# Optimization experiments

Hardware: AMD Instinct MI355X
Metric: run time of the kernel (lower is better)

## Reference

```python
import jax, jax.numpy as jnp
import numpy as np

D_MODEL = 1024


def bitlinear(x, weight):
    # ternary quantization with straight-through estimator; forward value is w_q*scale
    scale = jnp.clip(jnp.mean(jnp.abs(weight), axis=1, keepdims=True), 1e-5, None)
    w_q = jnp.clip(jnp.round(weight / scale), -1.0, 1.0)
    w = weight + jax.lax.stop_gradient(w_q * scale - weight)
    return x @ w.T


def rmsnorm(x, w, eps=1e-6):
    return x * jax.lax.rsqrt(jnp.mean(x * x, axis=-1, keepdims=True) + eps) * w


def setup_inputs() -> dict:
    key = jax.random.key(0)
    ks = jax.random.split(key, 6)
    D = D_MODEL
    std = np.sqrt(2.0 / D)  # kaiming_normal fan_out
    return {
        "x": jax.random.normal(ks[0], (4, 4096, D), dtype=jnp.float32),
        "Wr": jax.random.normal(ks[1], (D, D), dtype=jnp.float32) * std,
        "Wk": jax.random.normal(ks[2], (D, D), dtype=jnp.float32) * std,
        "Wv": jax.random.normal(ks[3], (D, D), dtype=jnp.float32) * std,
        "Wo": jax.random.normal(ks[4], (D, D), dtype=jnp.float32) * std,
        "decay": jnp.ones((D,), dtype=jnp.float32) * 0.99,
        "ln_w": jnp.ones((D,), dtype=jnp.float32),
    }


def reference(x, Wr, Wk, Wv, Wo, decay, ln_w):
    B, T, D = x.shape
    r = jax.nn.sigmoid(bitlinear(x, Wr))
    k = bitlinear(x, Wk)
    v = bitlinear(x, Wv)
    dec = jax.nn.sigmoid(decay)                              # [D]
    kv = k * v                                               # [B,T,D]
    positions = jnp.arange(T, dtype=x.dtype)                 # [T]
    log_decay = jnp.log(jnp.clip(dec, 1e-7, None))           # [D]
    scale = jnp.exp(positions[:, None] * log_decay[None, :])  # [T,D]
    scaled = kv / jnp.clip(scale, 1e-10, None)[None]         # [B,T,D]
    cum = jnp.cumsum(scaled, axis=1)                         # [B,T,D]
    state = cum * scale[None]                                # [B,T,D]
    return bitlinear(rmsnorm(r * state, ln_w), Wo)
```

## Files before the change

### kernel.cpp

```cpp
#include <hip/hip_runtime.h>

typedef unsigned short u16;
typedef __attribute__((ext_vector_type(8))) short bf16x8;
typedef __attribute__((ext_vector_type(4))) float f32x4;
typedef __attribute__((ext_vector_type(4))) unsigned short u16x4;

#define DM 1024

__device__ __forceinline__ float bf2f(u16 u){
  union { unsigned int i; float f; } v; v.i = ((unsigned int)u)<<16; return v.f;
}
__device__ __forceinline__ u16 f2bf(float f){
  unsigned int x = __float_as_uint(f);
  return (u16)((x + 0x7FFFu + ((x>>16)&1u)) >> 16);
}

__global__ __launch_bounds__(256)
void quantize_w(const float* __restrict__ W0, const float* __restrict__ W1,
                const float* __restrict__ W2, const float* __restrict__ W3,
                u16* __restrict__ wq, float* __restrict__ wsc)
{
  const int gr   = blockIdx.x*4 + (threadIdx.x>>6);
  const int lane = threadIdx.x & 63;
  const float* W; int row;
  if (gr < 1024)      { W = W0; row = gr; }
  else if (gr < 3072) { row = (gr-1024)>>1; W = (gr&1) ? W2 : W1; }
  else                { W = W3; row = gr-3072; }
  const float* wr = W + (size_t)row*DM;
  float4 v[4]; float s = 0.f;
  #pragma unroll
  for (int c=0;c<4;c++){
    v[c] = *(const float4*)&wr[c*256 + lane*4];
    s += fabsf(v[c].x)+fabsf(v[c].y)+fabsf(v[c].z)+fabsf(v[c].w);
  }
  #pragma unroll
  for (int off=32; off; off>>=1) s += __shfl_down(s, off);
  s = __shfl(s, 0);
  const float scale = fmaxf(s*(1.f/1024.f), 1e-5f);
  if (lane==0) wsc[gr] = scale;
  u16* wo = wq + (size_t)gr*DM;
  #pragma unroll
  for (int c=0;c<4;c++){
    u16x4 q;
    q[0] = f2bf(fminf(fmaxf(rintf(v[c].x/scale),-1.f),1.f));
    q[1] = f2bf(fminf(fmaxf(rintf(v[c].y/scale),-1.f),1.f));
    q[2] = f2bf(fminf(fmaxf(rintf(v[c].z/scale),-1.f),1.f));
    q[3] = f2bf(fminf(fmaxf(rintf(v[c].w/scale),-1.f),1.f));
    *(u16x4*)&wo[c*256 + lane*4] = q;
  }
}

__global__ void cvt_x(const float* __restrict__ x, u16* __restrict__ xb){
  const int i = (blockIdx.x*256 + threadIdx.x)*4;
  float4 v = *(const float4*)&x[i];
  u16x4 o; o[0]=f2bf(v.x); o[1]=f2bf(v.y); o[2]=f2bf(v.z); o[3]=f2bf(v.w);
  *(u16x4*)&xb[i] = o;
}


#define RD(base, off) (*(const bf16x8*)((const char*)(base) + (off)))

template<int MODE>
__global__ __launch_bounds__(256, 4)
void gemm_s(const u16* __restrict__ Ag, const u16* __restrict__ Bq,
            const float* __restrict__ bscale,
            u16* __restrict__ o_r, u16* __restrict__ o_kv,
            float* __restrict__ o_f)
{
  __shared__ u16 sA[128*64];
  __shared__ u16 sB[128*64];
  const int tid = threadIdx.x, wave = tid>>6, lane = tid&63;
  const int lr = lane&15, lg = lane>>4;
  const int wm = wave>>1, wn = wave&1;
  const int bm0 = blockIdx.x*128, bn0 = blockIdx.y*128;
  constexpr int nt = 16;

  const int r8   = lane>>3;
  const int scol = ((lane&7)<<4) ^ (r8<<4);
  const size_t aoff = (size_t)(bm0 + wave*8 + r8)*2048 + scol;
  const size_t boff = (size_t)(bn0 + wave*8 + r8)*2048 + scol;
  const int ldst = wave*1024;

  const int S = (lr&7)<<4;
  const int koff0 = ((lg<<4)     ) ^ S;
  const int koff1 = (64 + (lg<<4)) ^ S;
  const int arow = (wm*64 + lr)*128;
  const int brow = (wn*64 + lr)*128;

  f32x4 acc[4][4];
  #pragma unroll
  for (int i=0;i<4;i++)
    #pragma unroll
    for (int j=0;j<4;j++) acc[i][j] = (f32x4){0.f,0.f,0.f,0.f};

  for (int t=0; t<nt; ++t){
    #pragma unroll
    for (int q=0;q<4;q++){
      __builtin_amdgcn_global_load_lds(
        (const __attribute__((address_space(1))) void*)((const char*)Ag + aoff + q*65536 + (size_t)t*128),
        (__attribute__((address_space(3))) void*)((char*)sA + ldst + q*4096), 16, 0, 0);
      __builtin_amdgcn_global_load_lds(
        (const __attribute__((address_space(1))) void*)((const char*)Bq + boff + q*65536 + (size_t)t*128),
        (__attribute__((address_space(3))) void*)((char*)sB + ldst + q*4096), 16, 0, 0);
    }
    __syncthreads();
    {
      bf16x8 a[4], b[4];
      #pragma unroll
      for (int m=0;m<4;m++) a[m] = RD(sA, arow + m*2048 + koff0);
      #pragma unroll
      for (int n=0;n<4;n++) b[n] = RD(sB, brow + n*2048 + koff0);
      #pragma unroll
      for (int m=0;m<4;m++)
        #pragma unroll
        for (int n=0;n<4;n++)
          acc[m][n] = __builtin_amdgcn_mfma_f32_16x16x32_bf16(a[m], b[n], acc[m][n], 0,0,0);
      #pragma unroll
      for (int m=0;m<4;m++) a[m] = RD(sA, arow + m*2048 + koff1);
      #pragma unroll
      for (int n=0;n<4;n++) b[n] = RD(sB, brow + n*2048 + koff1);
      #pragma unroll
      for (int m=0;m<4;m++)
        #pragma unroll
        for (int n=0;n<4;n++)
          acc[m][n] = __builtin_amdgcn_mfma_f32_16x16x32_bf16(a[m], b[n], acc[m][n], 0,0,0);
    }
    __syncthreads();
  }

  #pragma unroll
  for (int mi=0; mi<4; ++mi){
    #pragma unroll
    for (int ni=0; ni<4; ++ni){
      const int col = bn0 + wn*64 + ni*16 + lr;
      const float sc = bscale[col];
      const int rowb = bm0 + wm*64 + mi*16 + lg*4;
      const f32x4 a = acc[mi][ni];
      if (MODE==0){
        if (bn0 < 1024){
          #pragma unroll
          for (int r2=0;r2<4;r2++){
            const float val = a[r2]*sc;
            o_r[(size_t)(rowb+r2)*DM + col] = f2bf(1.f/(1.f+expf(-val)));
          }
        } else {
          const int dv = (col - 1024) >> 1;
          #pragma unroll
          for (int r2=0;r2<4;r2++){
            const float val = a[r2]*sc;
            const float pr  = val * __shfl_xor(val, 1);
            if (!(lr & 1))
              o_kv[(size_t)(rowb+r2)*DM + dv] = f2bf(pr);
          }
        }
      } else {
        #pragma unroll
        for (int r2=0;r2<4;r2++)
          o_f[(size_t)(rowb+r2)*DM + col] = a[r2]*sc;
      }
    }
  }
}

__global__ __launch_bounds__(256)
void kv_phase1(const u16* __restrict__ kv, const float* __restrict__ decay,
               float* __restrict__ part)
{
  const int c = blockIdx.x & 127, b = blockIdx.x >> 7;
  const int d0 = threadIdx.x*4;
  float ld[4]; f32x4 sum = {0.f,0.f,0.f,0.f};
  #pragma unroll
  for (int j=0;j<4;j++){
    const float dec = 1.f/(1.f+expf(-decay[d0+j]));
    ld[j] = logf(fmaxf(dec, 1e-7f));
  }
  for (int t=c*32; t<c*32+32; ++t){
    const size_t base = ((size_t)(b*4096 + t))*DM + d0;
    const u16x4 p4 = *(const u16x4*)&kv[base];
    const float tf = (float)t;
    #pragma unroll
    for (int j=0;j<4;j++){
      const float e = expf(tf*ld[j]);
      sum[j] += bf2f(p4[j]) / fmaxf(e, 1e-10f);
    }
  }
  *(f32x4*)&part[((size_t)(b*128+c))*DM + d0] = sum;
}

__global__ void chunk_prefix(float* __restrict__ part){
  const int g = blockIdx.x*256 + threadIdx.x;
  const int b = g >> 8, d0 = (g & 255)*4;
  f32x4 run = {0.f,0.f,0.f,0.f};
  for (int c8=0; c8<128; c8+=8){
    f32x4 v[8];
    #pragma unroll
    for (int i=0;i<8;i++)
      v[i] = *(const f32x4*)&part[((size_t)(b*128+c8+i))*DM + d0];
    #pragma unroll
    for (int i=0;i<8;i++){
      const f32x4 tmp = v[i];
      *(f32x4*)&part[((size_t)(b*128+c8+i))*DM + d0] = run;
      run += tmp;
    }
  }
}

__global__ __launch_bounds__(256)
void scan_norm(const u16* __restrict__ kv, const u16* __restrict__ rbuf,
               const float* __restrict__ part, const float* __restrict__ decay,
               const float* __restrict__ lnw, u16* __restrict__ yn)
{
  const int c = blockIdx.x & 127, b = blockIdx.x >> 7;
  const int tid = threadIdx.x, lane = tid&63, wave = tid>>6;
  const int d0 = tid*4;
  __shared__ float red[2][4];
  f32x4 run = *(const f32x4*)&part[((size_t)(b*128+c))*DM + d0];
  float ld[4], lw[4];
  #pragma unroll
  for (int j=0;j<4;j++){
    const float dec = 1.f/(1.f+expf(-decay[d0+j]));
    ld[j] = logf(fmaxf(dec, 1e-7f));
    lw[j] = lnw[d0+j];
  }
  for (int t=c*32; t<c*32+32; ++t){
    const size_t base = ((size_t)(b*4096+t))*DM + d0;
    const u16x4 p4 = *(const u16x4*)&kv[base];
    const u16x4 r4 = *(const u16x4*)&rbuf[base];
    const float tf = (float)t;
    float y[4]; float ss = 0.f;
    #pragma unroll
    for (int j=0;j<4;j++){
      const float e = expf(tf*ld[j]);
      run[j] += bf2f(p4[j]) / fmaxf(e, 1e-10f);
      const float st = run[j]*e;
      y[j] = bf2f(r4[j])*st;
      ss += y[j]*y[j];
    }
    #pragma unroll
    for (int off=32; off; off>>=1) ss += __shfl_down(ss, off);
    if (lane==0) red[t&1][wave] = ss;
    __builtin_amdgcn_s_barrier();
    const float tot = (red[t&1][0]+red[t&1][1])+(red[t&1][2]+red[t&1][3]);
    const float rs = 1.f/sqrtf(tot*(1.f/1024.f) + 1e-6f);
    u16x4 o;
    #pragma unroll
    for (int j=0;j<4;j++) o[j] = f2bf(y[j]*rs*lw[j]);
    *(u16x4*)&yn[base] = o;
  }
}

extern "C" void kernel_launch(void* const* d_in, const int* in_sizes, int n_in,
                              void* d_out, int out_size, void* d_ws, size_t ws_size,
                              hipStream_t stream)
{
  (void)in_sizes; (void)n_in; (void)out_size; (void)ws_size;
  const float* x    = (const float*)d_in[0];
  const float* Wr   = (const float*)d_in[1];
  const float* Wk   = (const float*)d_in[2];
  const float* Wv   = (const float*)d_in[3];
  const float* Wo   = (const float*)d_in[4];
  const float* dec  = (const float*)d_in[5];
  const float* lnw  = (const float*)d_in[6];

  char* ws = (char*)d_ws;
  u16*   wq     = (u16*)(ws + 0);
  float* wsc    = (float*)(ws + 8388608);
  u16*   rbuf   = (u16*)(ws + 8404992);
  u16*   kvbuf  = (u16*)(ws + 41959424);
  float* part   = (float*)(ws + 75513856);
  u16*   xb     = (u16*)(ws + 77611008);
  u16*   yn     = (u16*)(ws + 111165440);

  quantize_w<<<1024, 256, 0, stream>>>(Wr, Wk, Wv, Wo, wq, wsc);
  cvt_x<<<16384, 256, 0, stream>>>(x, xb);
  gemm_s<0><<<dim3(128,24), 256, 0, stream>>>(xb, wq, wsc, rbuf, kvbuf, nullptr);
  kv_phase1<<<512, 256, 0, stream>>>(kvbuf, dec, part);
  chunk_prefix<<<4, 256, 0, stream>>>(part);
  scan_norm<<<512, 256, 0, stream>>>(kvbuf, rbuf, part, dec, lnw, yn);
  gemm_s<1><<<dim3(128,8), 256, 0, stream>>>(yn, wq + 3*1024*1024, wsc + 3072,
                                             nullptr, nullptr, (float*)d_out);
}
```

Baseline: 242.2 us.

## Quantize normalized activations to int8 and run output projection with int8 MFMA

The output projection now uses int8 ternary weights and per-row absmax int8-quantized activations, produced directly by the scan/norm kernel along with a per-row scale. It runs on a new int8 MFMA GEMM (16x16x64) with half the bytes per K step. The aim is to cut the final GEMM's load traffic and MFMA count and to shrink the yn write. It also widens the chunk prefix kernel to one scalar column per thread across more blocks. The cost is extra quantization error on activations (int8 vs bf16), which could affect tolerance.

```diff
diff --git a/kernel.cpp b/kernel.cpp
--- a/kernel.cpp
+++ b/kernel.cpp
@@ -3,6 +3,7 @@
 typedef unsigned short u16;
 typedef __attribute__((ext_vector_type(8))) short bf16x8;
 typedef __attribute__((ext_vector_type(4))) float f32x4;
+typedef __attribute__((ext_vector_type(4))) int   i32x4;
 typedef __attribute__((ext_vector_type(4))) unsigned short u16x4;
 
 #define DM 1024
@@ -18,7 +19,8 @@
 __global__ __launch_bounds__(256)
 void quantize_w(const float* __restrict__ W0, const float* __restrict__ W1,
                 const float* __restrict__ W2, const float* __restrict__ W3,
-                u16* __restrict__ wq, float* __restrict__ wsc)
+                u16* __restrict__ wq, signed char* __restrict__ wq8,
+                float* __restrict__ wsc)
 {
   const int gr   = blockIdx.x*4 + (threadIdx.x>>6);
   const int lane = threadIdx.x & 63;
@@ -38,15 +40,28 @@
   s = __shfl(s, 0);
   const float scale = fmaxf(s*(1.f/1024.f), 1e-5f);
   if (lane==0) wsc[gr] = scale;
-  u16* wo = wq + (size_t)gr*DM;
-  #pragma unroll
-  for (int c=0;c<4;c++){
-    u16x4 q;
-    q[0] = f2bf(fminf(fmaxf(rintf(v[c].x/scale),-1.f),1.f));
-    q[1] = f2bf(fminf(fmaxf(rintf(v[c].y/scale),-1.f),1.f));
-    q[2] = f2bf(fminf(fmaxf(rintf(v[c].z/scale),-1.f),1.f));
-    q[3] = f2bf(fminf(fmaxf(rintf(v[c].w/scale),-1.f),1.f));
-    *(u16x4*)&wo[c*256 + lane*4] = q;
+  if (gr < 3072){
+    u16* wo = wq + (size_t)gr*DM;
+    #pragma unroll
+    for (int c=0;c<4;c++){
+      u16x4 q;
+      q[0] = f2bf(fminf(fmaxf(rintf(v[c].x/scale),-1.f),1.f));
+      q[1] = f2bf(fminf(fmaxf(rintf(v[c].y/scale),-1.f),1.f));
+      q[2] = f2bf(fminf(fmaxf(rintf(v[c].z/scale),-1.f),1.f));
+      q[3] = f2bf(fminf(fmaxf(rintf(v[c].w/scale),-1.f),1.f));
+      *(u16x4*)&wo[c*256 + lane*4] = q;
+    }
+  } else {
+    signed char* wo = wq8 + (size_t)(gr-3072)*DM;
+    #pragma unroll
+    for (int c=0;c<4;c++){
+      const int q0 = (int)rintf(fminf(fmaxf(v[c].x/scale,-1.f),1.f));
+      const int q1 = (int)rintf(fminf(fmaxf(v[c].y/scale,-1.f),1.f));
+      const int q2 = (int)rintf(fminf(fmaxf(v[c].z/scale,-1.f),1.f));
+      const int q3 = (int)rintf(fminf(fmaxf(v[c].w/scale,-1.f),1.f));
+      const unsigned int p = (q0&0xFF) | ((q1&0xFF)<<8) | ((q2&0xFF)<<16) | ((unsigned)(q3&0xFF)<<24);
+      *(unsigned int*)&wo[c*256 + lane*4] = p;
+    }
   }
 }
 
@@ -57,15 +72,12 @@
   *(u16x4*)&xb[i] = o;
 }
 
-
 #define RD(base, off) (*(const bf16x8*)((const char*)(base) + (off)))
 
-template<int MODE>
 __global__ __launch_bounds__(256, 4)
-void gemm_s(const u16* __restrict__ Ag, const u16* __restrict__ Bq,
-            const float* __restrict__ bscale,
-            u16* __restrict__ o_r, u16* __restrict__ o_kv,
-            float* __restrict__ o_f)
+void gemm_rkv(const u16* __restrict__ Ag, const u16* __restrict__ Bq,
+              const float* __restrict__ bscale,
+              u16* __restrict__ o_r, u16* __restrict__ o_kv)
 {
   __shared__ u16 sA[128*64];
   __shared__ u16 sB[128*64];
@@ -136,28 +148,108 @@
       const float sc = bscale[col];
       const int rowb = bm0 + wm*64 + mi*16 + lg*4;
       const f32x4 a = acc[mi][ni];
-      if (MODE==0){
-        if (bn0 < 1024){
-          #pragma unroll
-          for (int r2=0;r2<4;r2++){
-            const float val = a[r2]*sc;
-            o_r[(size_t)(rowb+r2)*DM + col] = f2bf(1.f/(1.f+expf(-val)));
-          }
-        } else {
-          const int dv = (col - 1024) >> 1;
-          #pragma unroll
-          for (int r2=0;r2<4;r2++){
-            const float val = a[r2]*sc;
-            const float pr  = val * __shfl_xor(val, 1);
-            if (!(lr & 1))
-              o_kv[(size_t)(rowb+r2)*DM + dv] = f2bf(pr);
-          }
+      if (bn0 < 1024){
+        #pragma unroll
+        for (int r2=0;r2<4;r2++){
+          const float val = a[r2]*sc;
+          o_r[(size_t)(rowb+r2)*DM + col] = f2bf(1.f/(1.f+expf(-val)));
         }
       } else {
-        #pragma unroll
-        for (int r2=0;r2<4;r2++)
-          o_f[(size_t)(rowb+r2)*DM + col] = a[r2]*sc;
+        const int dv = (col - 1024) >> 1;
+        #pragma unroll
+        for (int r2=0;r2<4;r2++){
+          const float val = a[r2]*sc;
+          const float pr  = val * __shfl_xor(val, 1);
+          if (!(lr & 1))
+            o_kv[(size_t)(rowb+r2)*DM + dv] = f2bf(pr);
+        }
       }
+    }
+  }
+}
+
+#define RD8(base, off) (*(const i32x4*)((const char*)(base) + (off)))
+
+__global__ __launch_bounds__(256, 4)
+void gemm_o8(const signed char* __restrict__ Ag, const signed char* __restrict__ Bq,
+             const float* __restrict__ bscale, const float* __restrict__ sxr,
+             float* __restrict__ o_f)
+{
+  __shared__ signed char sA[128*128];
+  __shared__ signed char sB[128*128];
+  const int tid = threadIdx.x, wave = tid>>6, lane = tid&63;
+  const int lr = lane&15, lg = lane>>4;
+  const int wm = wave>>1, wn = wave&1;
+  const int bm0 = blockIdx.x*128, bn0 = blockIdx.y*128;
+  constexpr int nt = 8;
+
+  const int r8   = lane>>3;
+  const int scol = ((lane&7)<<4) ^ (r8<<4);
+  const size_t aoff = (size_t)(bm0 + wave*8 + r8)*1024 + scol;
+  const size_t boff = (size_t)(bn0 + wave*8 + r8)*1024 + scol;
+  const int ldst = wave*1024;
+
+  const int S = (lr&7)<<4;
+  const int koff0 = ((lg<<4)     ) ^ S;
+  const int koff1 = (64 + (lg<<4)) ^ S;
+  const int arow = (wm*64 + lr)*128;
+  const int brow = (wn*64 + lr)*128;
+
+  i32x4 acc[4][4];
+  #pragma unroll
+  for (int i=0;i<4;i++)
+    #pragma unroll
+    for (int j=0;j<4;j++) acc[i][j] = (i32x4){0,0,0,0};
+
+  for (int t=0; t<nt; ++t){
+    #pragma unroll
+    for (int q=0;q<4;q++){
+      __builtin_amdgcn_global_load_lds(
+        (const __attribute__((address_space(1))) void*)((const char*)Ag + aoff + q*32768 + (size_t)t*128),
+        (__attribute__((address_space(3))) void*)((char*)sA + ldst + q*4096), 16, 0, 0);
+      __builtin_amdgcn_global_load_lds(
+        (const __attribute__((address_space(1))) void*)((const char*)Bq + boff + q*32768 + (size_t)t*128),
+        (__attribute__((address_space(3))) void*)((char*)sB + ldst + q*4096), 16, 0, 0);
+    }
+    __syncthreads();
+    {
+      i32x4 a[4], b[4];
+      #pragma unroll
+      for (int m=0;m<4;m++) a[m] = RD8(sA, arow + m*2048 + koff0);
+      #pragma unroll
+      for (int n=0;n<4;n++) b[n] = RD8(sB, brow + n*2048 + koff0);
+      #pragma unroll
+      for (int m=0;m<4;m++)
+        #pragma unroll
+        for (int n=0;n<4;n++)
+          acc[m][n] = __builtin_amdgcn_mfma_i32_16x16x64_i8(a[m], b[n], acc[m][n], 0,0,0);
+      #pragma unroll
+      for (int m=0;m<4;m++) a[m] = RD8(sA, arow + m*2048 + koff1);
+      #pragma unroll
+      for (int n=0;n<4;n++) b[n] = RD8(sB, brow + n*2048 + koff1);
+      #pragma unroll
+      for (int m=0;m<4;m++)
+        #pragma unroll
+        for (int n=0;n<4;n++)
+          acc[m][n] = __builtin_amdgcn_mfma_i32_16x16x64_i8(a[m], b[n], acc[m][n], 0,0,0);
+    }
+    __syncthreads();
+  }
+
+  #pragma unroll
+  for (int mi=0; mi<4; ++mi){
+    const int rowb = bm0 + wm*64 + mi*16 + lg*4;
+    float sx[4];
+    #pragma unroll
+    for (int r2=0;r2<4;r2++) sx[r2] = sxr[rowb+r2];
+    #pragma unroll
+    for (int ni=0; ni<4; ++ni){
+      const int col = bn0 + wn*64 + ni*16 + lr;
+      const float sc = bscale[col];
+      const i32x4 a = acc[mi][ni];
+      #pragma unroll
+      for (int r2=0;r2<4;r2++)
+        o_f[(size_t)(rowb+r2)*DM + col] = (float)a[r2] * sx[r2] * sc;
     }
   }
 }
@@ -189,17 +281,17 @@
 
 __global__ void chunk_prefix(float* __restrict__ part){
   const int g = blockIdx.x*256 + threadIdx.x;
-  const int b = g >> 8, d0 = (g & 255)*4;
-  f32x4 run = {0.f,0.f,0.f,0.f};
+  const int b = g >> 10, d = g & 1023;
+  float run = 0.f;
   for (int c8=0; c8<128; c8+=8){
-    f32x4 v[8];
+    float v[8];
     #pragma unroll
     for (int i=0;i<8;i++)
-      v[i] = *(const f32x4*)&part[((size_t)(b*128+c8+i))*DM + d0];
+      v[i] = part[((size_t)(b*128+c8+i))*DM + d];
     #pragma unroll
     for (int i=0;i<8;i++){
-      const f32x4 tmp = v[i];
-      *(f32x4*)&part[((size_t)(b*128+c8+i))*DM + d0] = run;
+      const float tmp = v[i];
+      part[((size_t)(b*128+c8+i))*DM + d] = run;
       run += tmp;
     }
   }
@@ -208,12 +300,14 @@
 __global__ __launch_bounds__(256)
 void scan_norm(const u16* __restrict__ kv, const u16* __restrict__ rbuf,
                const float* __restrict__ part, const float* __restrict__ decay,
-               const float* __restrict__ lnw, u16* __restrict__ yn)
+               const float* __restrict__ lnw, signed char* __restrict__ yn8,
+               float* __restrict__ sxr)
 {
   const int c = blockIdx.x & 127, b = blockIdx.x >> 7;
   const int tid = threadIdx.x, lane = tid&63, wave = tid>>6;
   const int d0 = tid*4;
-  __shared__ float red[2][4];
+  __shared__ float redS[2][4];
+  __shared__ float redM[2][4];
   f32x4 run = *(const f32x4*)&part[((size_t)(b*128+c))*DM + d0];
   float ld[4], lw[4];
   #pragma unroll
@@ -227,25 +321,39 @@
     const u16x4 p4 = *(const u16x4*)&kv[base];
     const u16x4 r4 = *(const u16x4*)&rbuf[base];
     const float tf = (float)t;
-    float y[4]; float ss = 0.f;
+    float yl[4]; float ss = 0.f, mx = 0.f;
     #pragma unroll
     for (int j=0;j<4;j++){
       const float e = expf(tf*ld[j]);
       run[j] += bf2f(p4[j]) / fmaxf(e, 1e-10f);
       const float st = run[j]*e;
-      y[j] = bf2f(r4[j])*st;
-      ss += y[j]*y[j];
-    }
-    #pragma unroll
-    for (int off=32; off; off>>=1) ss += __shfl_down(ss, off);
-    if (lane==0) red[t&1][wave] = ss;
+      const float y = bf2f(r4[j])*st;
+      ss += y*y;
+      yl[j] = y*lw[j];
+      mx = fmaxf(mx, fabsf(yl[j]));
+    }
+    #pragma unroll
+    for (int off=32; off; off>>=1){
+      ss += __shfl_down(ss, off);
+      mx  = fmaxf(mx, __shfl_down(mx, off));
+    }
+    if (lane==0){ redS[t&1][wave] = ss; redM[t&1][wave] = mx; }
     __builtin_amdgcn_s_barrier();
-    const float tot = (red[t&1][0]+red[t&1][1])+(red[t&1][2]+red[t&1][3]);
-    const float rs = 1.f/sqrtf(tot*(1.f/1024.f) + 1e-6f);
-    u16x4 o;
-    #pragma unroll
-    for (int j=0;j<4;j++) o[j] = f2bf(y[j]*rs*lw[j]);
-    *(u16x4*)&yn[base] = o;
+    const float tot = (redS[t&1][0]+redS[t&1][1])+(redS[t&1][2]+redS[t&1][3]);
+    const float m1  = fmaxf(fmaxf(redM[t&1][0],redM[t&1][1]),
+                            fmaxf(redM[t&1][2],redM[t&1][3]));
+    const float rs  = 1.f/sqrtf(tot*(1.f/1024.f) + 1e-6f);
+    const float m1s = fmaxf(m1, 1e-30f);
+    const float qk  = 127.f/m1s;
+    if (tid==0) sxr[b*4096+t] = m1s*rs*(1.f/127.f);
+    unsigned int p = 0;
+    #pragma unroll
+    for (int j=0;j<4;j++){
+      int q = (int)rintf(yl[j]*qk);
+      q = q>127?127:(q<-127?-127:q);
+      p |= ((unsigned)(q&0xFF)) << (8*j);
+    }
+    *(unsigned int*)&yn8[base] = p;
   }
 }
 
@@ -263,20 +371,21 @@
   const float* lnw  = (const float*)d_in[6];
 
   char* ws = (char*)d_ws;
-  u16*   wq     = (u16*)(ws + 0);
-  float* wsc    = (float*)(ws + 8388608);
-  u16*   rbuf   = (u16*)(ws + 8404992);
-  u16*   kvbuf  = (u16*)(ws + 41959424);
-  float* part   = (float*)(ws + 75513856);
-  u16*   xb     = (u16*)(ws + 77611008);
-  u16*   yn     = (u16*)(ws + 111165440);
-
-  quantize_w<<<1024, 256, 0, stream>>>(Wr, Wk, Wv, Wo, wq, wsc);
+  u16*         wq    = (u16*)(ws + 0);
+  signed char* wq8   = (signed char*)(ws + 6291456);
+  float*       wsc   = (float*)(ws + 7340032);
+  u16*         rbuf  = (u16*)(ws + 7356416);
+  u16*         kvbuf = (u16*)(ws + 40910848);
+  float*       part  = (float*)(ws + 74465280);
+  u16*         xb    = (u16*)(ws + 76562432);
+  signed char* yn8   = (signed char*)(ws + 110116864);
+  float*       sxr   = (float*)(ws + 126894080);
+
+  quantize_w<<<1024, 256, 0, stream>>>(Wr, Wk, Wv, Wo, wq, wq8, wsc);
   cvt_x<<<16384, 256, 0, stream>>>(x, xb);
-  gemm_s<0><<<dim3(128,24), 256, 0, stream>>>(xb, wq, wsc, rbuf, kvbuf, nullptr);
+  gemm_rkv<<<dim3(128,24), 256, 0, stream>>>(xb, wq, wsc, rbuf, kvbuf);
   kv_phase1<<<512, 256, 0, stream>>>(kvbuf, dec, part);
-  chunk_prefix<<<4, 256, 0, stream>>>(part);
-  scan_norm<<<512, 256, 0, stream>>>(kvbuf, rbuf, part, dec, lnw, yn);
-  gemm_s<1><<<dim3(128,8), 256, 0, stream>>>(yn, wq + 3*1024*1024, wsc + 3072,
-                                             nullptr, nullptr, (float*)d_out);
-}
+  chunk_prefix<<<16, 256, 0, stream>>>(part);
+  scan_norm<<<512, 256, 0, stream>>>(kvbuf, rbuf, part, dec, lnw, yn8, sxr);
+  gemm_o8<<<dim3(128,8), 256, 0, stream>>>(yn8, wq8, wsc + 3072, sxr, (float*)d_out);
+}
```

New measurement: 221.6 us. 1.09x faster.
